# Kernel optimization log

Hardware: AMD Instinct MI355X
Metric: run time of the kernel (lower is better)

Reference implementation:

```python
import jax, jax.numpy as jnp
import numpy as np

EPS = 1.1920929e-07  # torch F.rms_norm default eps for fp32
HEADS = 16
KV_HEADS = 4
HEAD_DIM = 64
WINDOW = 1024
NEG = -1e30

def rms_norm(x):
    return x * jax.lax.rsqrt(jnp.mean(x * x, axis=-1, keepdims=True) + EPS)

def rope_freqs(L, head_dim):
    half = head_dim // 2
    inv_freq = 1.0 / (10000.0 ** (jnp.arange(half, dtype=jnp.float32) / half))
    f = jnp.outer(jnp.arange(L, dtype=jnp.float32), inv_freq)  # (L, half)
    return jnp.concatenate([f, f], axis=-1)  # (L, head_dim)

def apply_rope(x, freqs):
    # x: (B, L, H, D), freqs: (L, D)
    cos = jnp.cos(freqs)[None, :, None, :]
    sin = jnp.sin(freqs)[None, :, None, :]
    half = x.shape[-1] // 2
    x1, x2 = x[..., :half], x[..., half:]
    return jnp.concatenate([
        x1 * cos[..., :half] - x2 * sin[..., half:],
        x1 * sin[..., :half] + x2 * cos[..., half:],
    ], axis=-1)

def setup_inputs() -> dict:
    key = jax.random.key(0)
    k1, k2, k3, k4 = jax.random.split(key, 4)
    B, L, D = 2, 2048, 1024
    x = jax.random.normal(k1, (B, L, D), dtype=jnp.float32)
    w_qkv = jax.random.normal(k2, (1536, D), dtype=jnp.float32) * 0.02
    w_out = jax.random.normal(k3, (D, D), dtype=jnp.float32) * 0.02
    reset_mask = jax.random.randint(k4, (B, L), 0, 2) == 1
    return {"x": x, "w_qkv": w_qkv, "w_out": w_out, "reset_mask": reset_mask}

def reference(x, w_qkv, w_out, reset_mask):
    B, L, D = x.shape
    residual = x
    h = rms_norm(x)
    qkv = h @ w_qkv.T  # (B, L, 1536)
    q_dim = HEADS * HEAD_DIM
    kv_dim = KV_HEADS * HEAD_DIM
    q = qkv[..., :q_dim].reshape(B, L, HEADS, HEAD_DIM)
    k = qkv[..., q_dim:q_dim + kv_dim].reshape(B, L, KV_HEADS, HEAD_DIM)
    v = qkv[..., q_dim + kv_dim:].reshape(B, L, KV_HEADS, HEAD_DIM)
    q = rms_norm(q)
    k = rms_norm(k)
    freqs = rope_freqs(L, HEAD_DIM)
    q = apply_rope(q, freqs)
    k = apply_rope(k, freqs)
    groups = HEADS // KV_HEADS
    k = jnp.repeat(k, groups, axis=2)  # (B, L, H, D)
    v = jnp.repeat(v, groups, axis=2)
    q = q.transpose(0, 2, 1, 3)  # (B, H, L, D)
    k = k.transpose(0, 2, 1, 3)
    v = v.transpose(0, 2, 1, 3)
    # mask: same document & causal & sliding window
    seg = jnp.cumsum(reset_mask.astype(jnp.int32), axis=1)  # (B, L)
    same_doc = seg[:, :, None] == seg[:, None, :]  # (B, L, L)
    idx = jnp.arange(L)
    dist = idx[:, None] - idx[None, :]
    cw = (dist >= 0) & (dist < WINDOW)  # (L, L)
    mask = same_doc & cw[None]  # (B, L, L)
    scale = 1.0 / np.sqrt(HEAD_DIM)
    scores = jnp.einsum('bhqd,bhkd->bhqk', q, k) * scale
    scores = jnp.where(mask[:, None, :, :], scores, NEG)
    probs = jax.nn.softmax(scores, axis=-1)
    y = jnp.einsum('bhqk,bhkd->bhqd', probs, v)
    y = y.transpose(0, 2, 1, 3).reshape(B, L, D)
    return residual + y @ w_out.T
```

## Files before the change

### kernel.cpp

```cpp
#include <hip/hip_runtime.h>

typedef __attribute__((ext_vector_type(8))) short short8;
typedef __attribute__((ext_vector_type(4))) float f32x4;
typedef __attribute__((ext_vector_type(4))) unsigned short us4;

typedef unsigned int __attribute__((address_space(3))) lds_u32;
typedef const unsigned int __attribute__((address_space(1))) glb_u32;

__device__ __forceinline__ unsigned short f2bf(float f){
  unsigned int u = __float_as_uint(f);
  u = (u + 0x7FFFu + ((u >> 16) & 1u)) >> 16;
  return (unsigned short)u;
}
__device__ __forceinline__ float bf2f(unsigned short h){
  return __uint_as_float(((unsigned int)h) << 16);
}

__global__ __launch_bounds__(256)
void prep(const float* __restrict__ wq, const float* __restrict__ wo,
          unsigned short* __restrict__ wqb, unsigned short* __restrict__ wob,
          const float* __restrict__ x, unsigned short* __restrict__ h,
          const unsigned char* __restrict__ mb, int* __restrict__ lo){
  int blk = blockIdx.x;
  int t = threadIdx.x;
  if (blk < 2560) {
    int i = blk * 256 + t;
    const int n1 = 1536 * 1024 / 4;
    float4 v = (i < n1) ? ((const float4*)wq)[i] : ((const float4*)wo)[i - n1];
    us4 o = { f2bf(v.x), f2bf(v.y), f2bf(v.z), f2bf(v.w) };
    if (i < n1) ((us4*)wqb)[i] = o;
    else        ((us4*)wob)[i - n1] = o;
    return;
  }
  if (blk < 2560 + 4096) {
    int row = blk - 2560;
    float4 v = ((const float4*)(x + (size_t)row * 1024))[t];
    float ss = v.x*v.x + v.y*v.y + v.z*v.z + v.w*v.w;
    #pragma unroll
    for (int m = 1; m < 64; m <<= 1) ss += __shfl_xor(ss, m);
    __shared__ float wsum[4];
    if ((t & 63) == 0) wsum[t >> 6] = ss;
    __syncthreads();
    float tot = wsum[0] + wsum[1] + wsum[2] + wsum[3];
    float sc = rsqrtf(tot * (1.f/1024.f) + 1.1920929e-07f);
    us4 o = { f2bf(v.x*sc), f2bf(v.y*sc), f2bf(v.z*sc), f2bf(v.w*sc) };
    *(us4*)(h + (size_t)row * 1024 + t * 4) = o;
    return;
  }
  int b = blk - 2560 - 4096;
  __shared__ int flag_s;
  if (t == 0) flag_s = 0;
  __syncthreads();
  if (t < 64 && (t & 3) != 0 && mb[t] != 0) atomicOr(&flag_s, 1);
  __syncthreads();
  const bool isb = (flag_s != 0);
  const int* mi = (const int*)mb;
  int tmax = 0;
  int mvals[8];
  #pragma unroll
  for (int j = 0; j < 8; j++) {
    int p = t * 8 + j;
    int mv = isb ? (int)mb[b*2048 + p] : mi[b*2048 + p];
    mvals[j] = mv;
    if (mv) tmax = p;
  }
  __shared__ int sm[256];
  sm[t] = tmax;
  __syncthreads();
  for (int offd = 1; offd < 256; offd <<= 1) {
    int v = (t >= offd) ? sm[t - offd] : 0;
    __syncthreads();
    if (t >= offd) sm[t] = max(sm[t], v);
    __syncthreads();
  }
  int run = (t > 0) ? sm[t - 1] : 0;
  #pragma unroll
  for (int j = 0; j < 8; j++) {
    int p = t * 8 + j;
    if (mvals[j]) run = p;
    int l = run, wlo = p - 1023;
    if (wlo > l) l = wlo;
    if (l < 0) l = 0;
    lo[b*2048 + p] = l;
  }
}

template<bool BF_OUT, bool RES>
__global__ __launch_bounds__(256)
void gemm_nt(const unsigned short* __restrict__ A, const unsigned short* __restrict__ B,
             int M, int N, int K, float* __restrict__ Cf, unsigned short* __restrict__ Cb,
             const float* __restrict__ resid){
  __shared__ __align__(16) short As[128 * 64];
  __shared__ __align__(16) short Bs[128 * 64];
  const int nbn = N >> 7;
  const int bm = blockIdx.x / nbn;
  const int bn = blockIdx.x % nbn;
  const int t = threadIdx.x;
  const int lane = t & 63;
  const int wv = t >> 6;
  const int wm = (wv >> 1) * 64, wn = (wv & 1) * 64;
  const int lr = lane & 15, lg = lane >> 4;
  const int l8 = lane >> 3;
  const int c8 = (lane & 7) * 8;

  f32x4 acc[4][4];
  #pragma unroll
  for (int m = 0; m < 4; m++)
    #pragma unroll
    for (int n = 0; n < 4; n++) acc[m][n] = (f32x4){0.f,0.f,0.f,0.f};

  const unsigned short* Ab = A + (size_t)(bm * 128) * K;
  const unsigned short* Bb = B + (size_t)(bn * 128) * K;

  for (int kt = 0; kt < K; kt += 64) {
    #pragma unroll
    for (int i = 0; i < 4; i++) {
      int chunk = wv * 4 + i;
      int row = chunk * 8 + l8;
      __builtin_amdgcn_global_load_lds((glb_u32*)(Ab + (size_t)row * K + kt + c8),
                                       (lds_u32*)&As[chunk * 512], 16, 0, 0);
      __builtin_amdgcn_global_load_lds((glb_u32*)(Bb + (size_t)row * K + kt + c8),
                                       (lds_u32*)&Bs[chunk * 512], 16, 0, 0);
    }
    __syncthreads();
    #pragma unroll
    for (int kk = 0; kk < 2; kk++) {
      short8 af[4], bfr[4];
      #pragma unroll
      for (int m = 0; m < 4; m++) af[m] = *(const short8*)&As[(wm + m*16 + lr)*64 + kk*32 + lg*8];
      #pragma unroll
      for (int n = 0; n < 4; n++) bfr[n] = *(const short8*)&Bs[(wn + n*16 + lr)*64 + kk*32 + lg*8];
      #pragma unroll
      for (int m = 0; m < 4; m++)
        #pragma unroll
        for (int n = 0; n < 4; n++)
          acc[m][n] = __builtin_amdgcn_mfma_f32_16x16x32_bf16(af[m], bfr[n], acc[m][n], 0, 0, 0);
    }
    __syncthreads();
  }
  #pragma unroll
  for (int m = 0; m < 4; m++)
    #pragma unroll
    for (int n = 0; n < 4; n++)
      #pragma unroll
      for (int r = 0; r < 4; r++) {
        int grow = bm*128 + wm + m*16 + lg*4 + r;
        int gcol = bn*128 + wn + n*16 + lr;
        size_t idx = (size_t)grow * N + gcol;
        if (BF_OUT) { Cb[idx] = f2bf(acc[m][n][r]); }
        else {
          float v = acc[m][n][r];
          if (RES) v += resid[idx];
          Cf[idx] = v;
        }
      }
}

__global__ __launch_bounds__(256)
void post_qkv(const unsigned short* __restrict__ qkv,
              unsigned short* __restrict__ Qb, unsigned short* __restrict__ Kb,
              unsigned short* __restrict__ Vt){
  int w = blockIdx.x * 4 + (threadIdx.x >> 6);
  int lane = threadIdx.x & 63;
  int head = w % 24;
  int row  = w / 24;
  int b = row >> 11, pos = row & 2047;
  int off = head < 16 ? head * 64 : (head < 20 ? 1024 + (head-16)*64 : 1280 + (head-20)*64);
  float val = bf2f(qkv[(size_t)row * 1536 + off + lane]);
  if (head < 20) {
    float ss = val * val;
    #pragma unroll
    for (int m = 1; m < 64; m <<= 1) ss += __shfl_xor(ss, m);
    val *= rsqrtf(ss * (1.f/64.f) + 1.1920929e-07f);
    float part = __shfl_xor(val, 32);
    int i = lane & 31;
    float f = (float)pos * exp2f((float)i * (-13.287712379549449f / 32.f));
    float s, c; sincosf(f, &s, &c);
    val = (lane < 32) ? (val * c - part * s) : (part * s + val * c);
  }
  unsigned short o = f2bf(val);
  if (head < 16)      Qb[((size_t)((b*16 + head     )*2048 + pos))*64 + lane] = o;
  else if (head < 20) Kb[((size_t)((b*4  + head - 16)*2048 + pos))*64 + lane] = o;
  else                Vt[((size_t)((b*4  + head - 20)*64 + lane))*2048 + pos] = o;
}

__global__ __launch_bounds__(256)
void attn(const unsigned short* __restrict__ Qb, const unsigned short* __restrict__ Kb,
          const unsigned short* __restrict__ Vt, const int* __restrict__ lo,
          unsigned short* __restrict__ Y){
  int blk = blockIdx.x;
  int qt = blk & 31, h = (blk >> 5) & 15, b = blk >> 9;
  int wv = threadIdx.x >> 6, lane = threadIdx.x & 63;
  int lr = lane & 15, lg = lane >> 4;
  int q0 = qt * 64 + wv * 16;
  const unsigned short* Qh = Qb + ((size_t)(b*16 + h)) * 2048 * 64;
  int kvh = h >> 2;
  const unsigned short* Kh = Kb + ((size_t)(b*4 + kvh)) * 2048 * 64;
  const unsigned short* Vh = Vt + ((size_t)(b*4 + kvh)) * 64 * 2048;
  short8 qa0 = *(const short8*)(Qh + (size_t)(q0 + lr) * 64 + lg * 8);
  short8 qa1 = *(const short8*)(Qh + (size_t)(q0 + lr) * 64 + 32 + lg * 8);
  const int* lop = lo + b * 2048 + q0;
  int4 mlv = *(const int4*)(lop + lg * 4);
  int mylo[4] = {mlv.x, mlv.y, mlv.z, mlv.w};
  int kc0 = lop[0] & ~31;
  int kend = q0 + 15;
  f32x4 oacc[4];
  #pragma unroll
  for (int n = 0; n < 4; n++) oacc[n] = (f32x4){0.f,0.f,0.f,0.f};
  float den[4] = {0.f,0.f,0.f,0.f};
  __shared__ __align__(16) short Pl[4][16 * 40];
  short* Pw = Pl[wv];
  for (int kc = kc0; kc <= kend; kc += 32) {
    f32x4 s[2];
    #pragma unroll
    for (int n = 0; n < 2; n++) {
      int kr = kc + n*16 + lr;
      int krl = min(kr, 2047);
      short8 k0 = *(const short8*)(Kh + (size_t)krl * 64 + lg * 8);
      short8 k1 = *(const short8*)(Kh + (size_t)krl * 64 + 32 + lg * 8);
      f32x4 z = (f32x4){0.f,0.f,0.f,0.f};
      z = __builtin_amdgcn_mfma_f32_16x16x32_bf16(qa0, k0, z, 0, 0, 0);
      z = __builtin_amdgcn_mfma_f32_16x16x32_bf16(qa1, k1, z, 0, 0, 0);
      s[n] = z;
    }
    #pragma unroll
    for (int n = 0; n < 2; n++)
      #pragma unroll
      for (int r = 0; r < 4; r++) {
        int krow = kc + n*16 + lr;
        int qrow = q0 + lg*4 + r;
        bool valid = (krow >= mylo[r]) && (krow <= qrow);
        float p = valid ? __expf(s[n][r] * 0.125f) : 0.f;
        den[r] += p;
        Pw[(lg*4 + r) * 40 + n*16 + lr] = (short)f2bf(p);
      }
    short8 pa = *(const short8*)&Pw[lr * 40 + lg * 8];
    int vc = min(kc + lg * 8, 2040);
    #pragma unroll
    for (int n = 0; n < 4; n++) {
      short8 vb = *(const short8*)(Vh + (size_t)(n*16 + lr) * 2048 + vc);
      oacc[n] = __builtin_amdgcn_mfma_f32_16x16x32_bf16(pa, vb, oacc[n], 0, 0, 0);
    }
  }
  #pragma unroll
  for (int r = 0; r < 4; r++)
    #pragma unroll
    for (int m = 1; m < 16; m <<= 1) den[r] += __shfl_xor(den[r], m);
  #pragma unroll
  for (int n = 0; n < 4; n++)
    #pragma unroll
    for (int r = 0; r < 4; r++) {
      int qrow = q0 + lg*4 + r;
      Y[((size_t)(b*2048 + qrow)) * 1024 + h*64 + n*16 + lr] = f2bf(oacc[n][r] / den[r]);
    }
}

extern "C" void kernel_launch(void* const* d_in, const int* in_sizes, int n_in,
                              void* d_out, int out_size, void* d_ws, size_t ws_size,
                              hipStream_t stream){
  const float* x    = (const float*)d_in[0];
  const float* wqkv = (const float*)d_in[1];
  const float* wout = (const float*)d_in[2];
  const unsigned char* mask = (const unsigned char*)d_in[3];
  float* out = (float*)d_out;
  char* ws = (char*)d_ws;
  size_t off = 0;
  auto alloc = [&](size_t bytes) -> void* {
    void* p = ws + off;
    off += (bytes + 255) & ~(size_t)255;
    return p;
  };
  unsigned short* wq_b  = (unsigned short*)alloc((size_t)1536*1024*2);
  unsigned short* wo_b  = (unsigned short*)alloc((size_t)1024*1024*2);
  unsigned short* h_b   = (unsigned short*)alloc((size_t)4096*1024*2);
  unsigned short* qkv_b = (unsigned short*)alloc((size_t)4096*1536*2);
  unsigned short* q_b   = (unsigned short*)alloc((size_t)4096*1024*2);
  unsigned short* k_b   = (unsigned short*)alloc((size_t)4096*256*2);
  unsigned short* vt_b  = (unsigned short*)alloc((size_t)4096*256*2);
  unsigned short* y_b   = (unsigned short*)alloc((size_t)4096*1024*2);
  int* lo               = (int*)alloc((size_t)4096*4);

  prep<<<2560 + 4096 + 2, 256, 0, stream>>>(wqkv, wout, wq_b, wo_b, x, h_b, mask, lo);
  gemm_nt<true,  false><<<32*12, 256, 0, stream>>>(h_b, wq_b, 4096, 1536, 1024, nullptr, qkv_b, nullptr);
  post_qkv<<<24576, 256, 0, stream>>>(qkv_b, q_b, k_b, vt_b);
  attn<<<1024, 256, 0, stream>>>(q_b, k_b, vt_b, lo, y_b);
  gemm_nt<false, true><<<32*8, 256, 0, stream>>>(y_b, wo_b, 4096, 1024, 1024, out, nullptr, x);
}
```

Before: 164.8 us.

## Double-buffer GEMM LDS loads, swizzle block order, and rewrite QKV post-processing

The GEMM now double-buffers its A/B tiles in LDS, issuing the next K-tile's global-to-LDS loads before computing the current one, with explicit waitcnt and barriers to overlap memory with MFMA. Block indices are remapped by an XCD-style swizzle (groups of eight) to change cache locality across compute dies. The QKV post-processing kernel is rewritten so each wave handles two heads with packed 32-bit loads and stores. V is transposed through an LDS tile with vectorised stores instead of strided scalar writes. Risks are doubled LDS use lowering occupancy and hand-tuned waitcnt counts that assume exactly eight outstanding loads per stage.

```diff
diff --git a/kernel.cpp b/kernel.cpp
--- a/kernel.cpp
+++ b/kernel.cpp
@@ -90,11 +90,14 @@
 void gemm_nt(const unsigned short* __restrict__ A, const unsigned short* __restrict__ B,
              int M, int N, int K, float* __restrict__ Cf, unsigned short* __restrict__ Cb,
              const float* __restrict__ resid){
-  __shared__ __align__(16) short As[128 * 64];
-  __shared__ __align__(16) short Bs[128 * 64];
+  __shared__ __align__(16) short As[2][128 * 64];
+  __shared__ __align__(16) short Bs[2][128 * 64];
   const int nbn = N >> 7;
-  const int bm = blockIdx.x / nbn;
-  const int bn = blockIdx.x % nbn;
+  const int nwg = gridDim.x;
+  const int cpx = nwg >> 3;
+  const int swz = (blockIdx.x & 7) * cpx + (blockIdx.x >> 3);
+  const int bm = swz / nbn;
+  const int bn = swz % nbn;
   const int t = threadIdx.x;
   const int lane = t & 63;
   const int wv = t >> 6;
@@ -112,32 +115,54 @@
   const unsigned short* Ab = A + (size_t)(bm * 128) * K;
   const unsigned short* Bb = B + (size_t)(bn * 128) * K;
 
-  for (int kt = 0; kt < K; kt += 64) {
-    #pragma unroll
-    for (int i = 0; i < 4; i++) {
-      int chunk = wv * 4 + i;
-      int row = chunk * 8 + l8;
-      __builtin_amdgcn_global_load_lds((glb_u32*)(Ab + (size_t)row * K + kt + c8),
-                                       (lds_u32*)&As[chunk * 512], 16, 0, 0);
-      __builtin_amdgcn_global_load_lds((glb_u32*)(Bb + (size_t)row * K + kt + c8),
-                                       (lds_u32*)&Bs[chunk * 512], 16, 0, 0);
-    }
-    __syncthreads();
+  #define STAGE(buf, kt) do { \
+    _Pragma("unroll") \
+    for (int i = 0; i < 4; i++) { \
+      int chunk = wv * 4 + i; \
+      int row = chunk * 8 + l8; \
+      __builtin_amdgcn_global_load_lds((glb_u32*)(Ab + (size_t)row * K + (kt) + c8), \
+                                       (lds_u32*)&As[buf][chunk * 512], 16, 0, 0); \
+      __builtin_amdgcn_global_load_lds((glb_u32*)(Bb + (size_t)row * K + (kt) + c8), \
+                                       (lds_u32*)&Bs[buf][chunk * 512], 16, 0, 0); \
+    } \
+  } while (0)
+
+  auto COMPUTE = [&](int buf) {
     #pragma unroll
     for (int kk = 0; kk < 2; kk++) {
       short8 af[4], bfr[4];
       #pragma unroll
-      for (int m = 0; m < 4; m++) af[m] = *(const short8*)&As[(wm + m*16 + lr)*64 + kk*32 + lg*8];
-      #pragma unroll
-      for (int n = 0; n < 4; n++) bfr[n] = *(const short8*)&Bs[(wn + n*16 + lr)*64 + kk*32 + lg*8];
+      for (int m = 0; m < 4; m++) af[m] = *(const short8*)&As[buf][(wm + m*16 + lr)*64 + kk*32 + lg*8];
+      #pragma unroll
+      for (int n = 0; n < 4; n++) bfr[n] = *(const short8*)&Bs[buf][(wn + n*16 + lr)*64 + kk*32 + lg*8];
       #pragma unroll
       for (int m = 0; m < 4; m++)
         #pragma unroll
         for (int n = 0; n < 4; n++)
           acc[m][n] = __builtin_amdgcn_mfma_f32_16x16x32_bf16(af[m], bfr[n], acc[m][n], 0, 0, 0);
     }
-    __syncthreads();
-  }
+  };
+
+  const int nt = K >> 6;
+  STAGE(0, 0);
+  #pragma unroll 1
+  for (int tt = 0; tt < nt - 1; ++tt) {
+    int cur = tt & 1;
+    STAGE(cur ^ 1, (tt + 1) * 64);
+    __builtin_amdgcn_sched_barrier(0);
+    asm volatile("s_waitcnt vmcnt(8)" ::: "memory");
+    __builtin_amdgcn_s_barrier();
+    __builtin_amdgcn_sched_barrier(0);
+    COMPUTE(cur);
+    __builtin_amdgcn_sched_barrier(0);
+    __builtin_amdgcn_s_barrier();
+  }
+  asm volatile("s_waitcnt vmcnt(0)" ::: "memory");
+  __builtin_amdgcn_s_barrier();
+  __builtin_amdgcn_sched_barrier(0);
+  COMPUTE((nt - 1) & 1);
+  #undef STAGE
+
   #pragma unroll
   for (int m = 0; m < 4; m++)
     #pragma unroll
@@ -157,31 +182,71 @@
 }
 
 __global__ __launch_bounds__(256)
-void post_qkv(const unsigned short* __restrict__ qkv,
-              unsigned short* __restrict__ Qb, unsigned short* __restrict__ Kb,
-              unsigned short* __restrict__ Vt){
-  int w = blockIdx.x * 4 + (threadIdx.x >> 6);
-  int lane = threadIdx.x & 63;
-  int head = w % 24;
-  int row  = w / 24;
-  int b = row >> 11, pos = row & 2047;
-  int off = head < 16 ? head * 64 : (head < 20 ? 1024 + (head-16)*64 : 1280 + (head-20)*64);
-  float val = bf2f(qkv[(size_t)row * 1536 + off + lane]);
-  if (head < 20) {
-    float ss = val * val;
-    #pragma unroll
-    for (int m = 1; m < 64; m <<= 1) ss += __shfl_xor(ss, m);
-    val *= rsqrtf(ss * (1.f/64.f) + 1.1920929e-07f);
-    float part = __shfl_xor(val, 32);
-    int i = lane & 31;
-    float f = (float)pos * exp2f((float)i * (-13.287712379549449f / 32.f));
-    float s, c; sincosf(f, &s, &c);
-    val = (lane < 32) ? (val * c - part * s) : (part * s + val * c);
-  }
-  unsigned short o = f2bf(val);
-  if (head < 16)      Qb[((size_t)((b*16 + head     )*2048 + pos))*64 + lane] = o;
-  else if (head < 20) Kb[((size_t)((b*4  + head - 16)*2048 + pos))*64 + lane] = o;
-  else                Vt[((size_t)((b*4  + head - 20)*64 + lane))*2048 + pos] = o;
+void post2(const unsigned short* __restrict__ qkv,
+           unsigned short* __restrict__ Qb, unsigned short* __restrict__ Kb,
+           unsigned short* __restrict__ Vt){
+  __shared__ short Vl[64 * 72];
+  int blk = blockIdx.x;
+  int t = threadIdx.x;
+  if (blk < 10240) {
+    int w = blk * 4 + (t >> 6);
+    int lane = t & 63;
+    int row = w / 10, hp = w % 10;
+    int b = row >> 11, pos = row & 2047;
+    int ll = lane & 31, half = lane >> 5;
+    unsigned int pk = *(const unsigned int*)(qkv + (size_t)row * 1536 + hp * 128 + 2 * lane);
+    float v0 = bf2f((unsigned short)(pk & 0xFFFF));
+    float v1 = bf2f((unsigned short)(pk >> 16));
+    float ss = v0 * v0 + v1 * v1;
+    #pragma unroll
+    for (int m = 1; m < 32; m <<= 1) ss += __shfl_xor(ss, m);
+    float sc = rsqrtf(ss * (1.f/64.f) + 1.1920929e-07f);
+    v0 *= sc; v1 *= sc;
+    float p0 = __shfl_xor(v0, 16);
+    float p1 = __shfl_xor(v1, 16);
+    int i0 = 2 * (ll & 15);
+    const float cexp = -13.287712379549449f / 32.f;
+    float f0 = (float)pos * exp2f((float)i0 * cexp);
+    float f1 = (float)pos * exp2f((float)(i0 + 1) * cexp);
+    float s0, c0, s1, c1;
+    sincosf(f0, &s0, &c0);
+    sincosf(f1, &s1, &c1);
+    float o0, o1;
+    if (ll < 16) { o0 = v0 * c0 - p0 * s0; o1 = v1 * c1 - p1 * s1; }
+    else         { o0 = v0 * c0 + p0 * s0; o1 = v1 * c1 + p1 * s1; }
+    unsigned int opk = (unsigned int)f2bf(o0) | ((unsigned int)f2bf(o1) << 16);
+    if (hp < 8) {
+      int head = 2 * hp + half;
+      *(unsigned int*)(Qb + ((size_t)((b*16 + head) * 2048 + pos)) * 64 + 2 * ll) = opk;
+    } else {
+      int kvh = (hp - 8) * 2 + half;
+      *(unsigned int*)(Kb + ((size_t)((b*4 + kvh) * 2048 + pos)) * 64 + 2 * ll) = opk;
+    }
+    return;
+  }
+  int tb = blk - 10240;
+  int b = tb >> 7, kvh = (tb >> 5) & 3, pblk = tb & 31;
+  {
+    int r = t >> 2, cs = (t & 3) * 16;
+    int pos = pblk * 64 + r;
+    const unsigned short* src = qkv + ((size_t)(b*2048 + pos)) * 1536 + 1280 + kvh * 64 + cs;
+    short8 a0 = *(const short8*)(src);
+    short8 a1 = *(const short8*)(src + 8);
+    *(short8*)&Vl[r * 72 + cs]     = a0;
+    *(short8*)&Vl[r * 72 + cs + 8] = a1;
+  }
+  __syncthreads();
+  {
+    int d = t >> 2, ps = (t & 3) * 16;
+    short8 o0, o1;
+    #pragma unroll
+    for (int e = 0; e < 8; e++) o0[e] = Vl[(ps + e) * 72 + d];
+    #pragma unroll
+    for (int e = 0; e < 8; e++) o1[e] = Vl[(ps + 8 + e) * 72 + d];
+    unsigned short* dst = Vt + ((size_t)((b*4 + kvh) * 64 + d)) * 2048 + pblk * 64 + ps;
+    *(short8*)(dst)     = o0;
+    *(short8*)(dst + 8) = o1;
+  }
 }
 
 __global__ __launch_bounds__(256)
@@ -281,8 +346,8 @@
   int* lo               = (int*)alloc((size_t)4096*4);
 
   prep<<<2560 + 4096 + 2, 256, 0, stream>>>(wqkv, wout, wq_b, wo_b, x, h_b, mask, lo);
-  gemm_nt<true,  false><<<32*12, 256, 0, stream>>>(h_b, wq_b, 4096, 1536, 1024, nullptr, qkv_b, nullptr);
-  post_qkv<<<24576, 256, 0, stream>>>(qkv_b, q_b, k_b, vt_b);
+  gemm_nt<true,  false><<<384, 256, 0, stream>>>(h_b, wq_b, 4096, 1536, 1024, nullptr, qkv_b, nullptr);
+  post2<<<10240 + 256, 256, 0, stream>>>(qkv_b, q_b, k_b, vt_b);
   attn<<<1024, 256, 0, stream>>>(q_b, k_b, vt_b, lo, y_b);
-  gemm_nt<false, true><<<32*8, 256, 0, stream>>>(y_b, wo_b, 4096, 1024, 1024, out, nullptr, x);
-}
+  gemm_nt<false, true><<<256, 256, 0, stream>>>(y_b, wo_b, 4096, 1024, 1024, out, nullptr, x);
+}
```

After: 156.6 us. 4.9% less time.
